# Kernel optimization log

Measured on AMD Instinct MI355X. Metric: run time of the kernel, lower is better.

## Reference

```python
import jax, jax.numpy as jnp
import numpy as np

EMB = 1024
NUM_HEADS = 16


def setup_inputs() -> dict:
    key = jax.random.key(0)
    k_x, k_k, k_q, k_v, k_u, k_b = jax.random.split(key, 6)
    b, s, e = 4, 2048, EMB
    lim = 1.0 / np.sqrt(e)
    return {
        "x": jax.random.normal(k_x, (b, s, e), dtype=jnp.float32),
        "Wk": jax.random.uniform(k_k, (e, e), jnp.float32, -lim, lim),
        "Wq": jax.random.uniform(k_q, (e, e), jnp.float32, -lim, lim),
        "Wv": jax.random.uniform(k_v, (e, e), jnp.float32, -lim, lim),
        "Wu": jax.random.uniform(k_u, (e, e), jnp.float32, -lim, lim),
        "bu": jax.random.uniform(k_b, (e,), jnp.float32, -lim, lim),
    }


def reference(x, Wk, Wq, Wv, Wu, bu):
    b, s, e = x.shape
    h = NUM_HEADS
    d = e // h
    # scale q and k each by emb**(-1/4), as in the original (note: emb, not head_size)
    scale = e ** -0.25
    # project and split heads: (b, h, s, d)
    q = (x @ Wq.T).reshape(b, s, h, d).transpose(0, 2, 1, 3) * scale
    k = (x @ Wk.T).reshape(b, s, h, d).transpose(0, 2, 1, 3) * scale
    v = (x @ Wv.T).reshape(b, s, h, d).transpose(0, 2, 1, 3)
    # attention scores (b, h, s, s)
    dot = jnp.einsum("bhqd,bhkd->bhqk", q, k)
    # causal mask: strictly-upper triangle (offset=1) set to -inf
    causal = jnp.triu(jnp.ones((s, s), dtype=bool), k=1)
    dot = jnp.where(causal[None, None, :, :], -jnp.inf, dot)
    attn = jax.nn.softmax(dot, axis=-1)
    out = jnp.einsum("bhqk,bhkd->bhqd", attn, v)
    out = out.transpose(0, 2, 1, 3).reshape(b, s, e)
    return out @ Wu.T + bu
```

## Files before the change

kernel.cpp:

```cpp
#include <hip/hip_runtime.h>
#include <stdint.h>
#include <math.h>


typedef __attribute__((ext_vector_type(8))) short bf16x8;
typedef __attribute__((ext_vector_type(4))) float f32x4;
typedef __attribute__((ext_vector_type(16))) float f32x16;
typedef __attribute__((ext_vector_type(4))) int i32x4;
typedef __attribute__((ext_vector_type(4))) short s16x4;

#define GLOAD_LDS16(gp, lp)                                                     \
  __builtin_amdgcn_global_load_lds(                                             \
      (__attribute__((address_space(1))) void*)(gp),                            \
      (__attribute__((address_space(3))) void*)(lp), 16, 0, 0)

__device__ __forceinline__ short f2bf(float f) {
  union { float f; uint32_t u; } v; v.f = f;
  uint32_t r = v.u + 0x7FFFu + ((v.u >> 16) & 1u);
  return (short)(r >> 16);
}
__device__ __forceinline__ float bf2f(short s) {
  union { uint32_t u; float f; } v; v.u = ((uint32_t)(uint16_t)s) << 16;
  return v.f;
}
__device__ __forceinline__ short f2bfn(float f) {
  union { __bf16 h; short s; } u; u.h = (__bf16)f; return u.s;
}
__device__ __forceinline__ uint32_t pk2n(float a, float b) {
  union { __bf16 h[2]; uint32_t u; } v;
  v.h[0] = (__bf16)a; v.h[1] = (__bf16)b;
  return v.u;
}

__device__ __forceinline__ void swap32(uint32_t a, uint32_t b, int hi,
                                       uint32_t& out0, uint32_t& out1) {
#if __has_builtin(__builtin_amdgcn_permlane32_swap)
  typedef __attribute__((ext_vector_type(2))) int i32x2;
  i32x2 r = __builtin_amdgcn_permlane32_swap((int)a, (int)b, false, false);
  out0 = (uint32_t)r.x; out1 = (uint32_t)r.y;
#else
  uint32_t ta = (uint32_t)__shfl_xor((int)a, 32);
  uint32_t tb = (uint32_t)__shfl_xor((int)b, 32);
  out0 = hi ? tb : a;
  out1 = hi ? b : ta;
#endif
}

__global__ __launch_bounds__(256) void cast_kernel(const float* __restrict__ src,
                                                   short* __restrict__ dst, int n) {
  int i = (blockIdx.x * 256 + threadIdx.x) * 8;
  if (i >= n) return;
  const float4* s = (const float4*)(src + i);
  float4 f0 = s[0], f1 = s[1];
  bf16x8 o;
  o[0] = f2bf(f0.x); o[1] = f2bf(f0.y); o[2] = f2bf(f0.z); o[3] = f2bf(f0.w);
  o[4] = f2bf(f1.x); o[5] = f2bf(f1.y); o[6] = f2bf(f1.z); o[7] = f2bf(f1.w);
  *(bf16x8*)(dst + i) = o;
}

__global__ __launch_bounds__(256) void cast4_kernel(const float* __restrict__ w0,
                                                    const float* __restrict__ w1,
                                                    const float* __restrict__ w2,
                                                    const float* __restrict__ w3,
                                                    short* o0, short* o1, short* o2, short* o3) {
  const float* src = (blockIdx.y == 0) ? w0 : (blockIdx.y == 1) ? w1 : (blockIdx.y == 2) ? w2 : w3;
  short* dst = (blockIdx.y == 0) ? o0 : (blockIdx.y == 1) ? o1 : (blockIdx.y == 2) ? o2 : o3;
  int i = (blockIdx.x * 256 + threadIdx.x) * 8;
  const float4* s = (const float4*)(src + i);
  float4 f0 = s[0], f1 = s[1];
  bf16x8 o;
  o[0] = f2bf(f0.x); o[1] = f2bf(f0.y); o[2] = f2bf(f0.z); o[3] = f2bf(f0.w);
  o[4] = f2bf(f1.x); o[5] = f2bf(f1.y); o[6] = f2bf(f1.z); o[7] = f2bf(f1.w);
  *(bf16x8*)(dst + i) = o;
}

template <int MODE>
__device__ __forceinline__ void gemm_bt_core(short* __restrict__ a_lds,
                                             short* __restrict__ b_lds,
                                             const short* __restrict__ A,
                                             const short* __restrict__ Bm,
                                             short* __restrict__ Cb,
                                             float* __restrict__ Cf,
                                             const float* __restrict__ bias) {
  const float QSCALE = 0.03125f * 1.44269504f;
  const int tid = threadIdx.x;
  const int w = tid >> 6, l = tid & 63;
  const int l15 = l & 15, lhi = l >> 4;
  const int wr = w >> 1, wc = w & 1;
  const int row0 = blockIdx.x * 128;
  const int col0 = blockIdx.y * 128;

  f32x4 acc[4][4];
#pragma unroll
  for (int m = 0; m < 4; ++m)
#pragma unroll
    for (int n = 0; n < 4; ++n)
      acc[m][n] = (f32x4){0.f, 0.f, 0.f, 0.f};

  const int o0 = tid * 16;
  const int sr = o0 >> 7;
  const int sc = o0 & 127;

  for (int kt = 0; kt < 16; ++kt) {
    const char* Ab = (const char*)A + (size_t)(row0 + sr) * 2048 + kt * 128 + sc;
    const char* Bb = (const char*)Bm + (size_t)(col0 + sr) * 2048 + kt * 128 + sc;
#pragma unroll
    for (int i = 0; i < 4; ++i) {
      GLOAD_LDS16(Ab + (size_t)i * 32 * 2048, (char*)a_lds + i * 4096 + o0);
      GLOAD_LDS16(Bb + (size_t)i * 32 * 2048, (char*)b_lds + i * 4096 + o0);
    }
    __syncthreads();
#pragma unroll
    for (int kk = 0; kk < 2; ++kk) {
      bf16x8 af[4], bg[4];
#pragma unroll
      for (int m = 0; m < 4; ++m) {
        int r = wr * 64 + m * 16 + l15;
        af[m] = *(const bf16x8*)((const char*)a_lds + r * 128 + kk * 64 + lhi * 16);
      }
#pragma unroll
      for (int n = 0; n < 4; ++n) {
        int r = wc * 64 + n * 16 + l15;
        bg[n] = *(const bf16x8*)((const char*)b_lds + r * 128 + kk * 64 + lhi * 16);
      }
#pragma unroll
      for (int m = 0; m < 4; ++m)
#pragma unroll
        for (int n = 0; n < 4; ++n)
          acc[m][n] = __builtin_amdgcn_mfma_f32_16x16x32_bf16(af[m], bg[n], acc[m][n], 0, 0, 0);
    }
    __syncthreads();
  }

  if constexpr (MODE == 3) {
#pragma unroll
    for (int m = 0; m < 4; ++m)
#pragma unroll
      for (int n = 0; n < 4; ++n) {
        int colg = col0 + wc * 64 + n * 16 + l15;
#pragma unroll
        for (int r = 0; r < 4; ++r) {
          int rowg = row0 + wr * 64 + m * 16 + lhi * 4 + r;
          Cf[(size_t)rowg * 1024 + colg] = acc[m][n][r] + bias[colg];
        }
      }
  } else {
    const int bidx = row0 >> 11;
    const int hh = (col0 >> 6) + wc;
    const int t_base = ((row0 & 2047) + wr * 64) >> 5;
    const size_t base = ((size_t)(bidx * 16 + hh) * 64 + t_base) * 2048;
    if constexpr (MODE == 2) {
      const size_t c0 = base + (lhi >> 1) * 256 + l15 * 8 + (lhi & 1) * 4;
#pragma unroll
      for (int m = 0; m < 4; ++m)
#pragma unroll
        for (int n = 0; n < 4; ++n) {
          size_t idx = c0 + (size_t)(m >> 1) * 2048 + ((n >> 1) * 2 + (m & 1)) * 512 + (n & 1) * 128;
          s16x4 vv;
#pragma unroll
          for (int r = 0; r < 4; ++r) vv[r] = f2bfn(acc[m][n][r]);
          *(s16x4*)(Cb + idx) = vv;
        }
    } else {
      const size_t c0 = base + (l15 >> 3) * 256 + lhi * 32 + (l15 & 7);
#pragma unroll
      for (int m = 0; m < 4; ++m)
#pragma unroll
        for (int n = 0; n < 4; ++n) {
          size_t idx = c0 + (size_t)(m >> 1) * 2048 + n * 512 + (m & 1) * 128;
#pragma unroll
          for (int r = 0; r < 4; ++r)
            Cb[idx + r * 8] = f2bfn(MODE == 0 ? acc[m][n][r] * QSCALE : acc[m][n][r]);
        }
    }
  }
}

__global__ __launch_bounds__(256) void gemm_qkv_kernel(const short* __restrict__ xb,
                                                       const short* __restrict__ wq,
                                                       const short* __restrict__ wk,
                                                       const short* __restrict__ wv,
                                                       short* qf, short* kf, short* vf) {
  __shared__ short a_lds[128 * 64];
  __shared__ short b_lds[128 * 64];
  if (blockIdx.z == 0)      gemm_bt_core<0>(a_lds, b_lds, xb, wq, qf, nullptr, nullptr);
  else if (blockIdx.z == 1) gemm_bt_core<1>(a_lds, b_lds, xb, wk, kf, nullptr, nullptr);
  else                      gemm_bt_core<2>(a_lds, b_lds, xb, wv, vf, nullptr, nullptr);
}

__global__ __launch_bounds__(256) void gemm_out_kernel(const short* __restrict__ ob,
                                                       const short* __restrict__ wu,
                                                       const float* __restrict__ bias,
                                                       float* __restrict__ out) {
  __shared__ short a_lds[128 * 64];
  __shared__ short b_lds[128 * 64];
  gemm_bt_core<3>(a_lds, b_lds, ob, wu, nullptr, out, bias);
}

__global__ __launch_bounds__(512) void attn_kernel(const short* __restrict__ qf,
                                                   const short* __restrict__ kf,
                                                   const short* __restrict__ vf,
                                                   short* __restrict__ ob) {
  int bh = blockIdx.x;
  int b = bh >> 4, h = bh & 15;
  int tid = threadIdx.x;
  int wid = tid >> 6, l = tid & 63;
  int l31 = l & 31, hi = l >> 5;
  int pair = blockIdx.y * 4 + (wid >> 1);
  int team = wid & 1;
  int slot = wid >> 1;

  __shared__ float mrg[4][64][34];

  const short* qfb = qf + (size_t)bh * 131072;
  const short* kfb = kf + (size_t)bh * 131072;
  const short* vfb = vf + (size_t)bh * 131072;

  for (int part = 0; part < 2; ++part) {
    int sidx = part ? (63 - pair) : pair;
    int qrow0 = sidx * 32;
    int qg = qrow0 + l31;
    int n = sidx + 1;
    int t0 = team ? (n >> 1) : 0;
    int t1 = team ? n : (n >> 1);

    bf16x8 aq[4];
    {
      const short* qp = qfb + sidx * 2048 + l * 8;
#pragma unroll
      for (int s = 0; s < 4; ++s) aq[s] = *(const bf16x8*)(qp + s * 512);
    }

    f32x16 o_lo = {}, o_hi = {};
    float lsum = 0.f;

    if (t0 < t1) {
      const short* kp = kfb + (size_t)t0 * 2048 + l * 8;
      const short* vp = vfb + (size_t)t0 * 2048 + l * 8;
      bf16x8 kc[4];
#pragma unroll
      for (int s = 0; s < 4; ++s) kc[s] = *(const bf16x8*)(kp + s * 512);

      for (int t = t0; t < t1; ++t) {
        bf16x8 vc[4];
#pragma unroll
        for (int s = 0; s < 4; ++s) vc[s] = *(const bf16x8*)(vp + s * 512);
        vp += 2048;

        f32x16 st = {};
#pragma unroll
        for (int s = 0; s < 4; ++s)
          st = __builtin_amdgcn_mfma_f32_32x32x16_bf16(kc[s], aq[s], st, 0, 0, 0);

        kp += 2048;
        {
          const short* kpc = (t + 1 < t1) ? kp : (kp - 2048);
#pragma unroll
          for (int s = 0; s < 4; ++s) kc[s] = *(const bf16x8*)(kpc + s * 512);
        }

        if (t == sidx) {
#pragma unroll
          for (int r = 0; r < 16; ++r) {
            int kk = qrow0 + (r & 3) + 8 * (r >> 2) + 4 * hi;
            if (kk > qg) st[r] = -INFINITY;
          }
        }

#pragma unroll
        for (int r = 0; r < 16; ++r) st[r] = exp2f(st[r]);

        float sm[8];
#pragma unroll
        for (int r = 0; r < 8; ++r) sm[r] = st[r] + st[r + 8];
#pragma unroll
        for (int r = 0; r < 4; ++r) sm[r] += sm[r + 4];
        lsum += (sm[0] + sm[1]) + (sm[2] + sm[3]);

        uint32_t a0, a2, b1, b3, c0, c2, d1, d3;
        swap32(pk2n(st[0], st[1]),   pk2n(st[4], st[5]),   hi, a0, a2);
        swap32(pk2n(st[2], st[3]),   pk2n(st[6], st[7]),   hi, b1, b3);
        swap32(pk2n(st[8], st[9]),   pk2n(st[12], st[13]), hi, c0, c2);
        swap32(pk2n(st[10], st[11]), pk2n(st[14], st[15]), hi, d1, d3);
        i32x4 u0 = {(int)a0, (int)b1, (int)a2, (int)b3};
        i32x4 u1 = {(int)c0, (int)d1, (int)c2, (int)d3};
        bf16x8 pa0 = __builtin_bit_cast(bf16x8, u0);
        bf16x8 pa1 = __builtin_bit_cast(bf16x8, u1);

        o_lo = __builtin_amdgcn_mfma_f32_32x32x16_bf16(vc[0], pa0, o_lo, 0, 0, 0);
        o_lo = __builtin_amdgcn_mfma_f32_32x32x16_bf16(vc[1], pa1, o_lo, 0, 0, 0);
        o_hi = __builtin_amdgcn_mfma_f32_32x32x16_bf16(vc[2], pa0, o_hi, 0, 0, 0);
        o_hi = __builtin_amdgcn_mfma_f32_32x32x16_bf16(vc[3], pa1, o_hi, 0, 0, 0);
      }
    }

    lsum += __shfl_xor(lsum, 32);

    if (team == 1) {
      float* pp = &mrg[slot][l][0];
#pragma unroll
      for (int r = 0; r < 16; ++r) { pp[r] = o_lo[r]; pp[16 + r] = o_hi[r]; }
      pp[32] = lsum;
    }
    __syncthreads();
    if (team == 0) {
      const float* pp = &mrg[slot][l][0];
      float inv = 1.0f / (lsum + pp[32]);
      short* obase = ob + (size_t)(b * 2048 + qg) * 1024 + h * 64;
#pragma unroll
      for (int g = 0; g < 4; ++g) {
        int d0 = 8 * g + 4 * hi;
        s16x4 v0, v1;
#pragma unroll
        for (int jj = 0; jj < 4; ++jj) {
          v0[jj] = f2bfn((o_lo[4 * g + jj] + pp[4 * g + jj]) * inv);
          v1[jj] = f2bfn((o_hi[4 * g + jj] + pp[16 + 4 * g + jj]) * inv);
        }
        *(s16x4*)(obase + d0) = v0;
        *(s16x4*)(obase + 32 + d0) = v1;
      }
    }
    __syncthreads();
  }
}

extern "C" void kernel_launch(void* const* d_in, const int* in_sizes, int n_in,
                              void* d_out, int out_size, void* d_ws, size_t ws_size,
                              hipStream_t stream) {
  const float* x  = (const float*)d_in[0];
  const float* Wk = (const float*)d_in[1];
  const float* Wq = (const float*)d_in[2];
  const float* Wv = (const float*)d_in[3];
  const float* Wu = (const float*)d_in[4];
  const float* bu = (const float*)d_in[5];
  float* out = (float*)d_out;

  char* ws = (char*)d_ws;
  const size_t MB = 1u << 20;
  short* xb  = (short*)(ws + 0 * MB);
  short* qf  = (short*)(ws + 16 * MB);
  short* kfb = (short*)(ws + 32 * MB);
  short* vfb = (short*)(ws + 48 * MB);
  short* ob  = (short*)(ws + 64 * MB);
  short* wqb = (short*)(ws + 80 * MB);
  short* wkb = (short*)(ws + 82 * MB);
  short* wvb = (short*)(ws + 84 * MB);
  short* wub = (short*)(ws + 86 * MB);

  cast_kernel<<<4096, 256, 0, stream>>>(x, xb, 8388608);
  cast4_kernel<<<dim3(512, 4), 256, 0, stream>>>(Wq, Wk, Wv, Wu, wqb, wkb, wvb, wub);

  gemm_qkv_kernel<<<dim3(64, 8, 3), 256, 0, stream>>>(xb, wqb, wkb, wvb, qf, kfb, vfb);
  attn_kernel<<<dim3(64, 8), 512, 0, stream>>>(qf, kfb, vfb, ob);
  gemm_out_kernel<<<dim3(64, 8), 256, 0, stream>>>(ob, wub, bu, out);
}
```

Measured before the change: 175.4 us.

## Merge cast kernels, swizzle GEMM block order, raise MFMA wave priority

Folds the activation and weight bf16 casts into a single launch, which removes one kernel launch. Both GEMM kernels now use a 1D grid with a grouped row-block mapping: eight consecutive blocks share a column tile and span neighbouring row tiles, so A/B tiles are more likely to be reused from L2. The attention inner loop wraps its MFMA groups in s_setprio(1)/s_setprio(0) so waves issuing matrix ops get scheduling priority over waves doing exp and shuffle work. The remapping changes the per-XCD distribution of blocks, and the priority hints may have little effect.

After: 175.4 us. About the same (-0.0%).

```diff
diff --git a/kernel.cpp b/kernel.cpp
--- a/kernel.cpp
+++ b/kernel.cpp
@@ -46,26 +46,27 @@
 #endif
 }
 
-__global__ __launch_bounds__(256) void cast_kernel(const float* __restrict__ src,
-                                                   short* __restrict__ dst, int n) {
-  int i = (blockIdx.x * 256 + threadIdx.x) * 8;
-  if (i >= n) return;
-  const float4* s = (const float4*)(src + i);
-  float4 f0 = s[0], f1 = s[1];
-  bf16x8 o;
-  o[0] = f2bf(f0.x); o[1] = f2bf(f0.y); o[2] = f2bf(f0.z); o[3] = f2bf(f0.w);
-  o[4] = f2bf(f1.x); o[5] = f2bf(f1.y); o[6] = f2bf(f1.z); o[7] = f2bf(f1.w);
-  *(bf16x8*)(dst + i) = o;
-}
-
-__global__ __launch_bounds__(256) void cast4_kernel(const float* __restrict__ w0,
-                                                    const float* __restrict__ w1,
-                                                    const float* __restrict__ w2,
-                                                    const float* __restrict__ w3,
-                                                    short* o0, short* o1, short* o2, short* o3) {
-  const float* src = (blockIdx.y == 0) ? w0 : (blockIdx.y == 1) ? w1 : (blockIdx.y == 2) ? w2 : w3;
-  short* dst = (blockIdx.y == 0) ? o0 : (blockIdx.y == 1) ? o1 : (blockIdx.y == 2) ? o2 : o3;
-  int i = (blockIdx.x * 256 + threadIdx.x) * 8;
+__global__ __launch_bounds__(256) void cast_all_kernel(const float* __restrict__ x,
+                                                       const float* __restrict__ w0,
+                                                       const float* __restrict__ w1,
+                                                       const float* __restrict__ w2,
+                                                       const float* __restrict__ w3,
+                                                       short* __restrict__ xb,
+                                                       short* o0, short* o1, short* o2, short* o3) {
+  int bid = blockIdx.x;
+  const float* src;
+  short* dst;
+  int i;
+  if (bid < 4096) {
+    src = x; dst = xb;
+    i = (bid * 256 + threadIdx.x) * 8;
+  } else {
+    int r = bid - 4096;
+    int wsel = r >> 9, blk = r & 511;
+    src = (wsel == 0) ? w0 : (wsel == 1) ? w1 : (wsel == 2) ? w2 : w3;
+    dst = (wsel == 0) ? o0 : (wsel == 1) ? o1 : (wsel == 2) ? o2 : o3;
+    i = (blk * 256 + threadIdx.x) * 8;
+  }
   const float4* s = (const float4*)(src + i);
   float4 f0 = s[0], f1 = s[1];
   bf16x8 o;
@@ -81,14 +82,13 @@
                                              const short* __restrict__ Bm,
                                              short* __restrict__ Cb,
                                              float* __restrict__ Cf,
-                                             const float* __restrict__ bias) {
+                                             const float* __restrict__ bias,
+                                             int row0, int col0) {
   const float QSCALE = 0.03125f * 1.44269504f;
   const int tid = threadIdx.x;
   const int w = tid >> 6, l = tid & 63;
   const int l15 = l & 15, lhi = l >> 4;
   const int wr = w >> 1, wc = w & 1;
-  const int row0 = blockIdx.x * 128;
-  const int col0 = blockIdx.y * 128;
 
   f32x4 acc[4][4];
 #pragma unroll
@@ -183,9 +183,15 @@
                                                        short* qf, short* kf, short* vf) {
   __shared__ short a_lds[128 * 64];
   __shared__ short b_lds[128 * 64];
-  if (blockIdx.z == 0)      gemm_bt_core<0>(a_lds, b_lds, xb, wq, qf, nullptr, nullptr);
-  else if (blockIdx.z == 1) gemm_bt_core<1>(a_lds, b_lds, xb, wk, kf, nullptr, nullptr);
-  else                      gemm_bt_core<2>(a_lds, b_lds, xb, wv, vf, nullptr, nullptr);
+  int f = blockIdx.x;
+  int g = f & 7, j = f >> 3;
+  int rowb = g * 8 + (j & 7);
+  int cz = j >> 3;
+  int colb = cz & 7, z = cz >> 3;
+  int row0 = rowb * 128, col0 = colb * 128;
+  if (z == 0)      gemm_bt_core<0>(a_lds, b_lds, xb, wq, qf, nullptr, nullptr, row0, col0);
+  else if (z == 1) gemm_bt_core<1>(a_lds, b_lds, xb, wk, kf, nullptr, nullptr, row0, col0);
+  else             gemm_bt_core<2>(a_lds, b_lds, xb, wv, vf, nullptr, nullptr, row0, col0);
 }
 
 __global__ __launch_bounds__(256) void gemm_out_kernel(const short* __restrict__ ob,
@@ -194,7 +200,11 @@
                                                        float* __restrict__ out) {
   __shared__ short a_lds[128 * 64];
   __shared__ short b_lds[128 * 64];
-  gemm_bt_core<3>(a_lds, b_lds, ob, wu, nullptr, out, bias);
+  int f = blockIdx.x;
+  int g = f & 7, j = f >> 3;
+  int row0 = (g * 8 + (j & 7)) * 128;
+  int col0 = (j >> 3) * 128;
+  gemm_bt_core<3>(a_lds, b_lds, ob, wu, nullptr, out, bias, row0, col0);
 }
 
 __global__ __launch_bounds__(512) void attn_kernel(const short* __restrict__ qf,
@@ -248,9 +258,11 @@
         vp += 2048;
 
         f32x16 st = {};
+        __builtin_amdgcn_s_setprio(1);
 #pragma unroll
         for (int s = 0; s < 4; ++s)
           st = __builtin_amdgcn_mfma_f32_32x32x16_bf16(kc[s], aq[s], st, 0, 0, 0);
+        __builtin_amdgcn_s_setprio(0);
 
         kp += 2048;
         {
@@ -287,10 +299,12 @@
         bf16x8 pa0 = __builtin_bit_cast(bf16x8, u0);
         bf16x8 pa1 = __builtin_bit_cast(bf16x8, u1);
 
+        __builtin_amdgcn_s_setprio(1);
         o_lo = __builtin_amdgcn_mfma_f32_32x32x16_bf16(vc[0], pa0, o_lo, 0, 0, 0);
         o_lo = __builtin_amdgcn_mfma_f32_32x32x16_bf16(vc[1], pa1, o_lo, 0, 0, 0);
         o_hi = __builtin_amdgcn_mfma_f32_32x32x16_bf16(vc[2], pa0, o_hi, 0, 0, 0);
         o_hi = __builtin_amdgcn_mfma_f32_32x32x16_bf16(vc[3], pa1, o_hi, 0, 0, 0);
+        __builtin_amdgcn_s_setprio(0);
       }
     }
 
@@ -347,10 +361,8 @@
   short* wvb = (short*)(ws + 84 * MB);
   short* wub = (short*)(ws + 86 * MB);
 
-  cast_kernel<<<4096, 256, 0, stream>>>(x, xb, 8388608);
-  cast4_kernel<<<dim3(512, 4), 256, 0, stream>>>(Wq, Wk, Wv, Wu, wqb, wkb, wvb, wub);
-
-  gemm_qkv_kernel<<<dim3(64, 8, 3), 256, 0, stream>>>(xb, wqb, wkb, wvb, qf, kfb, vfb);
+  cast_all_kernel<<<6144, 256, 0, stream>>>(x, Wq, Wk, Wv, Wu, xb, wqb, wkb, wvb, wub);
+  gemm_qkv_kernel<<<1536, 256, 0, stream>>>(xb, wqb, wkb, wvb, qf, kfb, vfb);
   attn_kernel<<<dim3(64, 8), 512, 0, stream>>>(qf, kfb, vfb, ob);
-  gemm_out_kernel<<<dim3(64, 8), 256, 0, stream>>>(ob, wub, bu, out);
-}
+  gemm_out_kernel<<<512, 256, 0, stream>>>(ob, wub, bu, out);
+}
```
